# Kernel tuning notes

Hardware: AMD Instinct MI355X
Metric: run time of the kernel (lower is better)

The kernel has to match this reference:

```python
import jax, jax.numpy as jnp
import numpy as np

B, N, DIM = 4, 2048, 1024
HEADS, DIM_HEAD = 16, 64
INNER = HEADS * DIM_HEAD  # 1024
SCALE = DIM_HEAD ** -0.5

def setup_inputs() -> dict:
    key = jax.random.key(0)
    k1, k2, k3 = jax.random.split(key, 3)
    x = jax.random.normal(k1, (B, N, DIM), dtype=jnp.float32)
    w_qkv = jax.random.normal(k2, (DIM, 3 * INNER), dtype=jnp.float32) * (DIM ** -0.5)
    w_out = jax.random.normal(k3, (INNER, DIM), dtype=jnp.float32) * (INNER ** -0.5)
    b_out = jnp.zeros((DIM,), dtype=jnp.float32)
    return {"x": x, "w_qkv": w_qkv, "w_out": w_out, "b_out": b_out}

def reference(x, w_qkv, w_out, b_out):
    b, n, _ = x.shape
    qkv = x @ w_qkv  # [b, n, 3*inner]
    q, k, v = jnp.split(qkv, 3, axis=-1)
    # [b, n, h, d] -> [b, h, n, d]
    reshape = lambda t: t.reshape(b, n, HEADS, DIM_HEAD).transpose(0, 2, 1, 3)
    q, k, v = reshape(q), reshape(k), reshape(v)
    dots = jnp.einsum('bhqd,bhkd->bhqk', q, k) * SCALE
    attn = jax.nn.softmax(dots, axis=-1)
    out = jnp.einsum('bhqk,bhkd->bhqd', attn, v)
    out = out.transpose(0, 2, 1, 3).reshape(b, n, INNER)
    return out @ w_out + b_out
```

## Files before the change

kernel.cpp:

```cpp
#include <hip/hip_runtime.h>

typedef unsigned short u16;
typedef __bf16 bf16_t;
typedef bf16_t bf16x8 __attribute__((ext_vector_type(8)));
typedef float f32x4 __attribute__((ext_vector_type(4)));
typedef u16 u16x8 __attribute__((ext_vector_type(8)));
typedef u16 u16x4 __attribute__((ext_vector_type(4)));

#define B_     4
#define N_     2048
#define DIM_   1024
#define HEADS_ 16
#define DH_    64
#define INNER_ 1024
#define QKV3_  3072
#define SCALE_ 0.125f
#define LOG2E_ 1.44269504089f

__device__ __forceinline__ u16 f2bf(float f) {
  union { float f; unsigned u; } v; v.f = f;
  unsigned r = v.u + 0x7FFFu + ((v.u >> 16) & 1u);
  return (u16)(r >> 16);
}
__device__ __forceinline__ u16 bfbits(float f) {
  bf16_t b = (bf16_t)f;
  return __builtin_bit_cast(u16, b);
}

#if __has_builtin(__builtin_amdgcn_exp2f)
#define EXP2F(x) __builtin_amdgcn_exp2f(x)
#else
#define EXP2F(x) __expf((x) * 0.69314718056f)
#endif

typedef __attribute__((address_space(1))) const unsigned int ga_u32;
typedef __attribute__((address_space(3))) unsigned int ls_u32;
__device__ __forceinline__ void gload16(const void* g, void* l) {
  __builtin_amdgcn_global_load_lds((ga_u32*)g, (ls_u32*)l, 16, 0, 0);
}

__global__ __launch_bounds__(256) void cvt_f32_bf16(const float* __restrict__ in,
                                                    u16* __restrict__ out, int n8) {
  int i = blockIdx.x * 256 + threadIdx.x;
  if (i < n8) {
    const float4* p = (const float4*)(in + (size_t)i * 8);
    float4 a = p[0], b = p[1];
    u16x8 o;
    o[0] = f2bf(a.x); o[1] = f2bf(a.y); o[2] = f2bf(a.z); o[3] = f2bf(a.w);
    o[4] = f2bf(b.x); o[5] = f2bf(b.y); o[6] = f2bf(b.z); o[7] = f2bf(b.w);
    *(u16x8*)(out + (size_t)i * 8) = o;
  }
}

__global__ __launch_bounds__(256) void transp_w(const float* __restrict__ in,
                                                u16* __restrict__ out, int Kd, int Nd) {
  __shared__ float t[32][33];
  int n0 = blockIdx.x * 32, k0 = blockIdx.y * 32;
  int tx = threadIdx.x & 31, ty = threadIdx.x >> 5;
#pragma unroll
  for (int i = 0; i < 4; i++)
    t[ty + i * 8][tx] = in[(size_t)(k0 + ty + i * 8) * Nd + n0 + tx];
  __syncthreads();
#pragma unroll
  for (int i = 0; i < 4; i++)
    out[(size_t)(n0 + ty + i * 8) * Kd + k0 + tx] = f2bf(t[tx][ty + i * 8]);
}

__global__ __launch_bounds__(256) void transp_v(const u16* __restrict__ qkv,
                                                u16* __restrict__ vT) {
  __shared__ u16 t[32][33];
  int bh = blockIdx.z; int b = bh >> 4, h = bh & 15;
  int n0 = blockIdx.x * 32, d0 = blockIdx.y * 32;
  int tx = threadIdx.x & 31, ty = threadIdx.x >> 5;
#pragma unroll
  for (int i = 0; i < 4; i++)
    t[ty + i * 8][tx] =
        qkv[(size_t)(b * N_ + n0 + ty + i * 8) * QKV3_ + 2 * INNER_ + h * DH_ + d0 + tx];
  __syncthreads();
#pragma unroll
  for (int i = 0; i < 4; i++)
    vT[((size_t)bh * DH_ + d0 + ty + i * 8) * N_ + n0 + tx] = t[tx][ty + i * 8];
}

template <int F32OUT>
__global__ __launch_bounds__(256) void gemm_bt(const u16* __restrict__ A,
                                               const u16* __restrict__ BT,
                                               void* __restrict__ Cp,
                                               const float* __restrict__ bias,
                                               int M, int N, int K) {
  __shared__ alignas(16) u16 ldsA[128 * 64];
  __shared__ alignas(16) u16 ldsB[128 * 64];
  const int tid = threadIdx.x;
  const int lane = tid & 63, wid = tid >> 6;
  const int l16 = lane & 15, lg = lane >> 4;
  const int ntiles = N >> 7;
  const int tm = blockIdx.x / ntiles, tn = blockIdx.x % ntiles;
  const int m0 = tm << 7, n0 = tn << 7;
  const int wr = wid >> 1, wc = wid & 1;

  const int srow_in = lane >> 3;
  const int soff = ((lane & 7) ^ srow_in) * 8;

  f32x4 acc[4][4];
#pragma unroll
  for (int i = 0; i < 4; i++)
#pragma unroll
    for (int j = 0; j < 4; j++) acc[i][j] = f32x4{0.f, 0.f, 0.f, 0.f};

  for (int k0 = 0; k0 < K; k0 += 64) {
#pragma unroll
    for (int i = 0; i < 4; i++) {
      const int rbase = wid * 32 + i * 8;
      gload16(A  + (size_t)(m0 + rbase + srow_in) * K + k0 + soff,
              (char*)ldsA + rbase * 128);
      gload16(BT + (size_t)(n0 + rbase + srow_in) * K + k0 + soff,
              (char*)ldsB + rbase * 128);
    }
    __syncthreads();

    bf16x8 bf[4][2];
#pragma unroll
    for (int n = 0; n < 4; n++) {
      int row = wc * 64 + n * 16 + l16;
      int rb = row * 128, swz = (row & 7) << 4;
      bf[n][0] = *(const bf16x8*)((char*)ldsB + rb + ((lg * 16) ^ swz));
      bf[n][1] = *(const bf16x8*)((char*)ldsB + rb + ((64 + lg * 16) ^ swz));
    }
#pragma unroll
    for (int mm = 0; mm < 4; mm++) {
      int row = wr * 64 + mm * 16 + l16;
      int rb = row * 128, swz = (row & 7) << 4;
      bf16x8 af0 = *(const bf16x8*)((char*)ldsA + rb + ((lg * 16) ^ swz));
      bf16x8 af1 = *(const bf16x8*)((char*)ldsA + rb + ((64 + lg * 16) ^ swz));
#pragma unroll
      for (int n = 0; n < 4; n++) {
        acc[mm][n] = __builtin_amdgcn_mfma_f32_16x16x32_bf16(af0, bf[n][0], acc[mm][n], 0, 0, 0);
        acc[mm][n] = __builtin_amdgcn_mfma_f32_16x16x32_bf16(af1, bf[n][1], acc[mm][n], 0, 0, 0);
      }
    }
    __syncthreads();
  }

#pragma unroll
  for (int mm = 0; mm < 4; mm++) {
#pragma unroll
    for (int n = 0; n < 4; n++) {
      int row = m0 + wr * 64 + mm * 16 + lg * 4;
      int col = n0 + wc * 64 + n * 16 + l16;
#pragma unroll
      for (int j = 0; j < 4; j++) {
        if (F32OUT)
          ((float*)Cp)[(size_t)(row + j) * N + col] = acc[mm][n][j] + bias[col];
        else
          ((u16*)Cp)[(size_t)(row + j) * N + col] = f2bf(acc[mm][n][j]);
      }
    }
  }
}

__global__ __launch_bounds__(512, 4) void attn_fwd(const u16* __restrict__ qkv,
                                                   const u16* __restrict__ vT,
                                                   u16* __restrict__ abuf) {
  __shared__ alignas(16) u16 ldsK[2][64 * 64];
  __shared__ alignas(16) u16 ldsV[2][64 * 64];
  __shared__ alignas(16) u16 plds[8][32 * 64];

  const int tid = threadIdx.x;
  const int lane = tid & 63, wid = tid >> 6;
  const int l16 = lane & 15, lg = lane >> 4;

  int bid = blockIdx.x;
  bid = (bid & 7) * 64 + (bid >> 3);
  const int bh = bid >> 3, qt = bid & 7;
  const int b = bh >> 4, h = bh & 15;
  const int q0 = qt * 256 + wid * 32;

  bf16x8 qf[2][2];
#pragma unroll
  for (int mm = 0; mm < 2; mm++) {
    const u16* qrow = qkv + (size_t)(b * N_ + q0 + mm * 16 + l16) * QKV3_ + h * DH_;
    bf16x8 t0 = *(const bf16x8*)(qrow + lg * 8);
    bf16x8 t1 = *(const bf16x8*)(qrow + 32 + lg * 8);
#pragma unroll
    for (int i = 0; i < 8; i++) {
      t0[i] = (bf16_t)((float)t0[i] * SCALE_);
      t1[i] = (bf16_t)((float)t1[i] * SCALE_);
    }
    qf[mm][0] = t0; qf[mm][1] = t1;
  }

  const int srow = (wid << 3) + (lane >> 3);
  const int sswz = (lane & 7) ^ (srow & 7);
  const u16* ksrc = qkv + (size_t)(b * N_ + srow) * QKV3_ + INNER_ + h * DH_ + sswz * 8;
  const u16* vsrc = vT + ((size_t)bh * DH_ + srow) * N_ + sswz * 8;
  const int sdst = wid << 10;

  char* pwave = (char*)&plds[wid][0];

  float mrow[2], lrow[2];
  f32x4 acc[2][4];
#pragma unroll
  for (int mm = 0; mm < 2; mm++) { mrow[mm] = -1e30f; lrow[mm] = 0.f; }
#pragma unroll
  for (int mm = 0; mm < 2; mm++)
#pragma unroll
    for (int d = 0; d < 4; d++) acc[mm][d] = f32x4{0.f, 0.f, 0.f, 0.f};

  gload16(ksrc, (char*)&ldsK[0][0] + sdst);
  gload16(vsrc, (char*)&ldsV[0][0] + sdst);
  __syncthreads();

  const int NT = N_ / 64;
  for (int kt = 0; kt < NT; ++kt) {
    const int cur = kt & 1;
    if (kt < NT - 1) {
      gload16(ksrc + (size_t)(kt + 1) * 64 * QKV3_, (char*)&ldsK[cur ^ 1][0] + sdst);
      gload16(vsrc + (kt + 1) * 64, (char*)&ldsV[cur ^ 1][0] + sdst);
    }

    const char* Kb = (const char*)&ldsK[cur][0];
    const char* Vb = (const char*)&ldsV[cur][0];

    f32x4 s[2][4];
    __builtin_amdgcn_s_setprio(1);
#pragma unroll
    for (int kc = 0; kc < 4; kc++) {
      int r = kc * 16 + l16;
      const char* rb = Kb + r * 128;
      int swz = (r & 7) << 4;
      bf16x8 kf0 = *(const bf16x8*)(rb + ((lg * 16) ^ swz));
      bf16x8 kf1 = *(const bf16x8*)(rb + ((64 + lg * 16) ^ swz));
#pragma unroll
      for (int mm = 0; mm < 2; mm++) {
        f32x4 c = f32x4{0.f, 0.f, 0.f, 0.f};
        c = __builtin_amdgcn_mfma_f32_16x16x32_bf16(kf0, qf[mm][0], c, 0, 0, 0);
        c = __builtin_amdgcn_mfma_f32_16x16x32_bf16(kf1, qf[mm][1], c, 0, 0, 0);
        s[mm][kc] = c;
      }
    }
    __builtin_amdgcn_s_setprio(0);

#pragma unroll
    for (int mm = 0; mm < 2; mm++) {
      float t = fmaxf(fmaxf(fmaxf(s[mm][0][0], s[mm][0][1]), fmaxf(s[mm][0][2], s[mm][0][3])),
                      fmaxf(fmaxf(s[mm][1][0], s[mm][1][1]), fmaxf(s[mm][1][2], s[mm][1][3])));
      float u = fmaxf(fmaxf(fmaxf(s[mm][2][0], s[mm][2][1]), fmaxf(s[mm][2][2], s[mm][2][3])),
                      fmaxf(fmaxf(s[mm][3][0], s[mm][3][1]), fmaxf(s[mm][3][2], s[mm][3][3])));
      t = fmaxf(t, u);
      t = fmaxf(t, __shfl_xor(t, 16));
      t = fmaxf(t, __shfl_xor(t, 32));
      float mn = fmaxf(mrow[mm], t);
      if (__ballot(mn - mrow[mm] > 8.f)) {
        float alpha = __expf(mrow[mm] - mn);
        mrow[mm] = mn;
        lrow[mm] *= alpha;
#pragma unroll
        for (int dd = 0; dd < 4; dd++)
#pragma unroll
          for (int j = 0; j < 4; j++) acc[mm][dd][j] *= alpha;
      }
      const float nm2 = -mrow[mm] * LOG2E_;
      float psum = 0.f;
      int r = mm * 16 + l16;
      int swz = (r & 7) << 4;
#pragma unroll
      for (int kc = 0; kc < 4; kc++) {
        float p0 = EXP2F(__builtin_fmaf(s[mm][kc][0], LOG2E_, nm2));
        float p1 = EXP2F(__builtin_fmaf(s[mm][kc][1], LOG2E_, nm2));
        float p2 = EXP2F(__builtin_fmaf(s[mm][kc][2], LOG2E_, nm2));
        float p3 = EXP2F(__builtin_fmaf(s[mm][kc][3], LOG2E_, nm2));
        psum += (p0 + p1) + (p2 + p3);
        u16x4 w;
        w[0] = bfbits(p0); w[1] = bfbits(p1); w[2] = bfbits(p2); w[3] = bfbits(p3);
        *(u16x4*)(pwave + r * 128 + ((kc * 32 + lg * 8) ^ swz)) = w;
      }
      psum += __shfl_xor(psum, 16);
      psum += __shfl_xor(psum, 32);
      lrow[mm] += psum;
    }

    bf16x8 pa[2][2];
#pragma unroll
    for (int mm = 0; mm < 2; mm++) {
      int r = mm * 16 + l16;
      int swz = (r & 7) << 4;
#pragma unroll
      for (int ks = 0; ks < 2; ks++)
        pa[mm][ks] = *(const bf16x8*)(pwave + r * 128 + ((ks * 64 + lg * 16) ^ swz));
    }
    __builtin_amdgcn_s_setprio(1);
#pragma unroll
    for (int dd = 0; dd < 4; dd++) {
      int r = dd * 16 + l16;
      const char* rb = Vb + r * 128;
      int swz = (r & 7) << 4;
      bf16x8 vf0 = *(const bf16x8*)(rb + ((lg * 16) ^ swz));
      bf16x8 vf1 = *(const bf16x8*)(rb + ((64 + lg * 16) ^ swz));
#pragma unroll
      for (int mm = 0; mm < 2; mm++) {
        acc[mm][dd] = __builtin_amdgcn_mfma_f32_16x16x32_bf16(vf0, pa[mm][0], acc[mm][dd], 0, 0, 0);
        acc[mm][dd] = __builtin_amdgcn_mfma_f32_16x16x32_bf16(vf1, pa[mm][1], acc[mm][dd], 0, 0, 0);
      }
    }
    __builtin_amdgcn_s_setprio(0);

    __syncthreads();
  }

#pragma unroll
  for (int mm = 0; mm < 2; mm++) {
    float inv = 1.f / lrow[mm];
    size_t row = (size_t)(b * N_ + q0 + mm * 16 + l16);
#pragma unroll
    for (int dd = 0; dd < 4; dd++) {
      u16x4 w;
#pragma unroll
      for (int j = 0; j < 4; j++) w[j] = bfbits(acc[mm][dd][j] * inv);
      *(u16x4*)(abuf + row * INNER_ + h * DH_ + dd * 16 + lg * 4) = w;
    }
  }
}

extern "C" void kernel_launch(void* const* d_in, const int* in_sizes, int n_in,
                              void* d_out, int out_size, void* d_ws, size_t ws_size,
                              hipStream_t stream) {
  const float* x     = (const float*)d_in[0];
  const float* w_qkv = (const float*)d_in[1];
  const float* w_out = (const float*)d_in[2];
  const float* b_out = (const float*)d_in[3];
  float* out = (float*)d_out;

  char* ws = (char*)d_ws;
  u16* xb    = (u16*)(ws);
  u16* wqkvT = (u16*)(ws + (size_t)(16 << 20));
  u16* woutT = (u16*)(ws + (size_t)(22 << 20));
  u16* qkv   = (u16*)(ws + (size_t)(24 << 20));
  u16* vTb   = (u16*)(ws + (size_t)(72 << 20));
  u16* abuf  = xb;

  cvt_f32_bf16<<<4096, 256, 0, stream>>>(x, xb, (B_ * N_ * DIM_) / 8);
  transp_w<<<dim3(QKV3_ / 32, DIM_ / 32), 256, 0, stream>>>(w_qkv, wqkvT, DIM_, QKV3_);
  transp_w<<<dim3(DIM_ / 32, INNER_ / 32), 256, 0, stream>>>(w_out, woutT, INNER_, DIM_);
  gemm_bt<0><<<(B_ * N_ / 128) * (QKV3_ / 128), 256, 0, stream>>>(
      xb, wqkvT, qkv, nullptr, B_ * N_, QKV3_, DIM_);
  transp_v<<<dim3(N_ / 32, DH_ / 32, B_ * HEADS_), 256, 0, stream>>>(qkv, vTb);
  attn_fwd<<<512, 512, 0, stream>>>(qkv, vTb, abuf);
  gemm_bt<1><<<(B_ * N_ / 128) * (DIM_ / 128), 256, 0, stream>>>(
      abuf, woutT, out, b_out, B_ * N_, DIM_, INNER_);
}
```

Measured before the change: 210.8 us.

## Use 32x32x16 MFMA in attention with register P via permlane32 swap

Rewrites the attention kernel to use 32x32x16 bf16 MFMAs with one 32-row query tile per wave. The softmax probabilities now stay in registers and are rearranged into MFMA operand layout with permlane32_swap, which removes the per-wave P staging buffer in LDS and its store/load round trip. Blocks shrink to 4 waves (256 threads) and the grid doubles to 1024 blocks with an adjusted block-to-head swizzle. The cost is larger accumulator register footprint per thread and a dependence on the correctness of the permlane-based layout mapping.

```diff
diff --git a/kernel.cpp b/kernel.cpp
--- a/kernel.cpp
+++ b/kernel.cpp
@@ -4,8 +4,10 @@
 typedef __bf16 bf16_t;
 typedef bf16_t bf16x8 __attribute__((ext_vector_type(8)));
 typedef float f32x4 __attribute__((ext_vector_type(4)));
+typedef float f32x16 __attribute__((ext_vector_type(16)));
 typedef u16 u16x8 __attribute__((ext_vector_type(8)));
 typedef u16 u16x4 __attribute__((ext_vector_type(4)));
+typedef unsigned uint2v __attribute__((ext_vector_type(2)));
 
 #define B_     4
 #define N_     2048
@@ -25,6 +27,9 @@
 __device__ __forceinline__ u16 bfbits(float f) {
   bf16_t b = (bf16_t)f;
   return __builtin_bit_cast(u16, b);
+}
+__device__ __forceinline__ unsigned packbf(float lo, float hi) {
+  return (unsigned)bfbits(lo) | ((unsigned)bfbits(hi) << 16);
 }
 
 #if __has_builtin(__builtin_amdgcn_exp2f)
@@ -158,167 +163,161 @@
   }
 }
 
-__global__ __launch_bounds__(512, 4) void attn_fwd(const u16* __restrict__ qkv,
+__global__ __launch_bounds__(256, 4) void attn_fwd(const u16* __restrict__ qkv,
                                                    const u16* __restrict__ vT,
                                                    u16* __restrict__ abuf) {
   __shared__ alignas(16) u16 ldsK[2][64 * 64];
   __shared__ alignas(16) u16 ldsV[2][64 * 64];
-  __shared__ alignas(16) u16 plds[8][32 * 64];
 
   const int tid = threadIdx.x;
   const int lane = tid & 63, wid = tid >> 6;
-  const int l16 = lane & 15, lg = lane >> 4;
+  const int l32 = lane & 31, hl = lane >> 5;
 
   int bid = blockIdx.x;
-  bid = (bid & 7) * 64 + (bid >> 3);
-  const int bh = bid >> 3, qt = bid & 7;
+  bid = (bid & 7) * 128 + (bid >> 3);
+  const int bh = bid >> 4, qt = bid & 15;
   const int b = bh >> 4, h = bh & 15;
-  const int q0 = qt * 256 + wid * 32;
-
-  bf16x8 qf[2][2];
-#pragma unroll
-  for (int mm = 0; mm < 2; mm++) {
-    const u16* qrow = qkv + (size_t)(b * N_ + q0 + mm * 16 + l16) * QKV3_ + h * DH_;
-    bf16x8 t0 = *(const bf16x8*)(qrow + lg * 8);
-    bf16x8 t1 = *(const bf16x8*)(qrow + 32 + lg * 8);
-#pragma unroll
-    for (int i = 0; i < 8; i++) {
-      t0[i] = (bf16_t)((float)t0[i] * SCALE_);
-      t1[i] = (bf16_t)((float)t1[i] * SCALE_);
-    }
-    qf[mm][0] = t0; qf[mm][1] = t1;
-  }
-
-  const int srow = (wid << 3) + (lane >> 3);
-  const int sswz = (lane & 7) ^ (srow & 7);
+  const int q0 = qt * 128 + wid * 32;
+
+  bf16x8 qf[4];
+  {
+    const u16* qrow = qkv + (size_t)(b * N_ + q0 + l32) * QKV3_ + h * DH_ + hl * 8;
+#pragma unroll
+    for (int step = 0; step < 4; step++) {
+      bf16x8 t = *(const bf16x8*)(qrow + step * 16);
+#pragma unroll
+      for (int i = 0; i < 8; i++) t[i] = (bf16_t)((float)t[i] * SCALE_);
+      qf[step] = t;
+    }
+  }
+
+  const int srow = tid >> 3;
+  const int sswz = (tid & 7) ^ (srow & 7);
   const u16* ksrc = qkv + (size_t)(b * N_ + srow) * QKV3_ + INNER_ + h * DH_ + sswz * 8;
   const u16* vsrc = vT + ((size_t)bh * DH_ + srow) * N_ + sswz * 8;
-  const int sdst = wid << 10;
-
-  char* pwave = (char*)&plds[wid][0];
-
-  float mrow[2], lrow[2];
-  f32x4 acc[2][4];
-#pragma unroll
-  for (int mm = 0; mm < 2; mm++) { mrow[mm] = -1e30f; lrow[mm] = 0.f; }
-#pragma unroll
-  for (int mm = 0; mm < 2; mm++)
-#pragma unroll
-    for (int d = 0; d < 4; d++) acc[mm][d] = f32x4{0.f, 0.f, 0.f, 0.f};
-
-  gload16(ksrc, (char*)&ldsK[0][0] + sdst);
-  gload16(vsrc, (char*)&ldsV[0][0] + sdst);
+  const int sdst0 = wid << 10;
+  const int sdst1 = 4096 + (wid << 10);
+
+  float mrow = -1e30f, lrow = 0.f;
+  f32x16 acc[2];
+#pragma unroll
+  for (int i = 0; i < 16; i++) { acc[0][i] = 0.f; acc[1][i] = 0.f; }
+
+  gload16(ksrc, (char*)&ldsK[0][0] + sdst0);
+  gload16(ksrc + (size_t)32 * QKV3_, (char*)&ldsK[0][0] + sdst1);
+  gload16(vsrc, (char*)&ldsV[0][0] + sdst0);
+  gload16(vsrc + 32 * N_, (char*)&ldsV[0][0] + sdst1);
   __syncthreads();
 
   const int NT = N_ / 64;
   for (int kt = 0; kt < NT; ++kt) {
     const int cur = kt & 1;
     if (kt < NT - 1) {
-      gload16(ksrc + (size_t)(kt + 1) * 64 * QKV3_, (char*)&ldsK[cur ^ 1][0] + sdst);
-      gload16(vsrc + (kt + 1) * 64, (char*)&ldsV[cur ^ 1][0] + sdst);
+      const u16* kp = ksrc + (size_t)(kt + 1) * 64 * QKV3_;
+      const u16* vp = vsrc + (kt + 1) * 64;
+      gload16(kp, (char*)&ldsK[cur ^ 1][0] + sdst0);
+      gload16(kp + (size_t)32 * QKV3_, (char*)&ldsK[cur ^ 1][0] + sdst1);
+      gload16(vp, (char*)&ldsV[cur ^ 1][0] + sdst0);
+      gload16(vp + 32 * N_, (char*)&ldsV[cur ^ 1][0] + sdst1);
     }
 
     const char* Kb = (const char*)&ldsK[cur][0];
     const char* Vb = (const char*)&ldsV[cur][0];
 
-    f32x4 s[2][4];
+    f32x16 s[2];
     __builtin_amdgcn_s_setprio(1);
 #pragma unroll
-    for (int kc = 0; kc < 4; kc++) {
-      int r = kc * 16 + l16;
+    for (int ktile = 0; ktile < 2; ktile++) {
+      f32x16 c;
+#pragma unroll
+      for (int i = 0; i < 16; i++) c[i] = 0.f;
+      const int r = ktile * 32 + l32;
       const char* rb = Kb + r * 128;
-      int swz = (r & 7) << 4;
-      bf16x8 kf0 = *(const bf16x8*)(rb + ((lg * 16) ^ swz));
-      bf16x8 kf1 = *(const bf16x8*)(rb + ((64 + lg * 16) ^ swz));
-#pragma unroll
-      for (int mm = 0; mm < 2; mm++) {
-        f32x4 c = f32x4{0.f, 0.f, 0.f, 0.f};
-        c = __builtin_amdgcn_mfma_f32_16x16x32_bf16(kf0, qf[mm][0], c, 0, 0, 0);
-        c = __builtin_amdgcn_mfma_f32_16x16x32_bf16(kf1, qf[mm][1], c, 0, 0, 0);
-        s[mm][kc] = c;
-      }
+      const int swz = (r & 7) << 4;
+#pragma unroll
+      for (int step = 0; step < 4; step++) {
+        bf16x8 kf = *(const bf16x8*)(rb + ((step * 32 + hl * 16) ^ swz));
+        c = __builtin_amdgcn_mfma_f32_32x32x16_bf16(kf, qf[step], c, 0, 0, 0);
+      }
+      s[ktile] = c;
     }
     __builtin_amdgcn_s_setprio(0);
 
-#pragma unroll
-    for (int mm = 0; mm < 2; mm++) {
-      float t = fmaxf(fmaxf(fmaxf(s[mm][0][0], s[mm][0][1]), fmaxf(s[mm][0][2], s[mm][0][3])),
-                      fmaxf(fmaxf(s[mm][1][0], s[mm][1][1]), fmaxf(s[mm][1][2], s[mm][1][3])));
-      float u = fmaxf(fmaxf(fmaxf(s[mm][2][0], s[mm][2][1]), fmaxf(s[mm][2][2], s[mm][2][3])),
-                      fmaxf(fmaxf(s[mm][3][0], s[mm][3][1]), fmaxf(s[mm][3][2], s[mm][3][3])));
-      t = fmaxf(t, u);
-      t = fmaxf(t, __shfl_xor(t, 16));
-      t = fmaxf(t, __shfl_xor(t, 32));
-      float mn = fmaxf(mrow[mm], t);
-      if (__ballot(mn - mrow[mm] > 8.f)) {
-        float alpha = __expf(mrow[mm] - mn);
-        mrow[mm] = mn;
-        lrow[mm] *= alpha;
-#pragma unroll
-        for (int dd = 0; dd < 4; dd++)
-#pragma unroll
-          for (int j = 0; j < 4; j++) acc[mm][dd][j] *= alpha;
-      }
-      const float nm2 = -mrow[mm] * LOG2E_;
-      float psum = 0.f;
-      int r = mm * 16 + l16;
-      int swz = (r & 7) << 4;
-#pragma unroll
-      for (int kc = 0; kc < 4; kc++) {
-        float p0 = EXP2F(__builtin_fmaf(s[mm][kc][0], LOG2E_, nm2));
-        float p1 = EXP2F(__builtin_fmaf(s[mm][kc][1], LOG2E_, nm2));
-        float p2 = EXP2F(__builtin_fmaf(s[mm][kc][2], LOG2E_, nm2));
-        float p3 = EXP2F(__builtin_fmaf(s[mm][kc][3], LOG2E_, nm2));
-        psum += (p0 + p1) + (p2 + p3);
-        u16x4 w;
-        w[0] = bfbits(p0); w[1] = bfbits(p1); w[2] = bfbits(p2); w[3] = bfbits(p3);
-        *(u16x4*)(pwave + r * 128 + ((kc * 32 + lg * 8) ^ swz)) = w;
-      }
-      psum += __shfl_xor(psum, 16);
-      psum += __shfl_xor(psum, 32);
-      lrow[mm] += psum;
-    }
-
-    bf16x8 pa[2][2];
-#pragma unroll
-    for (int mm = 0; mm < 2; mm++) {
-      int r = mm * 16 + l16;
-      int swz = (r & 7) << 4;
-#pragma unroll
-      for (int ks = 0; ks < 2; ks++)
-        pa[mm][ks] = *(const bf16x8*)(pwave + r * 128 + ((ks * 64 + lg * 16) ^ swz));
-    }
+    float t0 = s[0][0];
+#pragma unroll
+    for (int i = 1; i < 16; i++) t0 = fmaxf(t0, s[0][i]);
+#pragma unroll
+    for (int i = 0; i < 16; i++) t0 = fmaxf(t0, s[1][i]);
+    t0 = fmaxf(t0, __shfl_xor(t0, 32));
+    const float mn = fmaxf(mrow, t0);
+    if (__ballot(mn - mrow > 8.f)) {
+      const float alpha = __expf(mrow - mn);
+      mrow = mn;
+      lrow *= alpha;
+#pragma unroll
+      for (int i = 0; i < 16; i++) { acc[0][i] *= alpha; acc[1][i] *= alpha; }
+    }
+    const float nm2 = -mrow * LOG2E_;
+    float psum = 0.f;
+#pragma unroll
+    for (int ktile = 0; ktile < 2; ktile++)
+#pragma unroll
+      for (int i = 0; i < 16; i++) {
+        const float p = EXP2F(__builtin_fmaf(s[ktile][i], LOG2E_, nm2));
+        s[ktile][i] = p;
+        psum += p;
+      }
+    psum += __shfl_xor(psum, 32);
+    lrow += psum;
+
+    bf16x8 pb[4];
+#pragma unroll
+    for (int ktile = 0; ktile < 2; ktile++)
+#pragma unroll
+      for (int par = 0; par < 2; par++) {
+        const int rb8 = par * 8;
+        const unsigned c0 = packbf(s[ktile][rb8 + 0], s[ktile][rb8 + 1]);
+        const unsigned c1 = packbf(s[ktile][rb8 + 2], s[ktile][rb8 + 3]);
+        const unsigned c2 = packbf(s[ktile][rb8 + 4], s[ktile][rb8 + 5]);
+        const unsigned c3 = packbf(s[ktile][rb8 + 6], s[ktile][rb8 + 7]);
+        const uint2v r02 = __builtin_amdgcn_permlane32_swap(c0, c2, false, false);
+        const uint2v r13 = __builtin_amdgcn_permlane32_swap(c1, c3, false, false);
+        union { unsigned u[4]; bf16x8 v; } w;
+        w.u[0] = r02[0]; w.u[1] = r13[0]; w.u[2] = r02[1]; w.u[3] = r13[1];
+        pb[ktile * 2 + par] = w.v;
+      }
+
     __builtin_amdgcn_s_setprio(1);
 #pragma unroll
-    for (int dd = 0; dd < 4; dd++) {
-      int r = dd * 16 + l16;
+    for (int dtile = 0; dtile < 2; dtile++) {
+      const int r = dtile * 32 + l32;
       const char* rb = Vb + r * 128;
-      int swz = (r & 7) << 4;
-      bf16x8 vf0 = *(const bf16x8*)(rb + ((lg * 16) ^ swz));
-      bf16x8 vf1 = *(const bf16x8*)(rb + ((64 + lg * 16) ^ swz));
-#pragma unroll
-      for (int mm = 0; mm < 2; mm++) {
-        acc[mm][dd] = __builtin_amdgcn_mfma_f32_16x16x32_bf16(vf0, pa[mm][0], acc[mm][dd], 0, 0, 0);
-        acc[mm][dd] = __builtin_amdgcn_mfma_f32_16x16x32_bf16(vf1, pa[mm][1], acc[mm][dd], 0, 0, 0);
-      }
+      const int swz = (r & 7) << 4;
+      f32x16 c = acc[dtile];
+#pragma unroll
+      for (int step = 0; step < 4; step++) {
+        bf16x8 vf = *(const bf16x8*)(rb + ((step * 32 + hl * 16) ^ swz));
+        c = __builtin_amdgcn_mfma_f32_32x32x16_bf16(vf, pb[step], c, 0, 0, 0);
+      }
+      acc[dtile] = c;
     }
     __builtin_amdgcn_s_setprio(0);
 
     __syncthreads();
   }
 
-#pragma unroll
-  for (int mm = 0; mm < 2; mm++) {
-    float inv = 1.f / lrow[mm];
-    size_t row = (size_t)(b * N_ + q0 + mm * 16 + l16);
-#pragma unroll
-    for (int dd = 0; dd < 4; dd++) {
+  const float inv = 1.f / lrow;
+  const size_t row = (size_t)(b * N_ + q0 + l32);
+#pragma unroll
+  for (int dtile = 0; dtile < 2; dtile++)
+#pragma unroll
+    for (int g = 0; g < 4; g++) {
       u16x4 w;
 #pragma unroll
-      for (int j = 0; j < 4; j++) w[j] = bfbits(acc[mm][dd][j] * inv);
-      *(u16x4*)(abuf + row * INNER_ + h * DH_ + dd * 16 + lg * 4) = w;
-    }
-  }
+      for (int j = 0; j < 4; j++) w[j] = bfbits(acc[dtile][g * 4 + j] * inv);
+      const int d = dtile * 32 + g * 8 + hl * 4;
+      *(u16x4*)(abuf + row * INNER_ + h * DH_ + d) = w;
+    }
 }
 
 extern "C" void kernel_launch(void* const* d_in, const int* in_sizes, int n_in,
@@ -344,7 +343,7 @@
   gemm_bt<0><<<(B_ * N_ / 128) * (QKV3_ / 128), 256, 0, stream>>>(
       xb, wqkvT, qkv, nullptr, B_ * N_, QKV3_, DIM_);
   transp_v<<<dim3(N_ / 32, DH_ / 32, B_ * HEADS_), 256, 0, stream>>>(qkv, vTb);
-  attn_fwd<<<512, 512, 0, stream>>>(qkv, vTb, abuf);
+  attn_fwd<<<1024, 256, 0, stream>>>(qkv, vTb, abuf);
   gemm_bt<1><<<(B_ * N_ / 128) * (DIM_ / 128), 256, 0, stream>>>(
       abuf, woutT, out, b_out, B_ * N_, DIM_, INNER_);
 }
```

Result: no change. 213.0 us (+1.1%).
